# Kernel tuning notes

Hardware: AMD Instinct MI355X
Metric: run time of the kernel (lower is better)

Reference implementation:

```python
import jax, jax.numpy as jnp
import numpy as np

B, S, D, H = 16, 1024, 512, 8
DH = D // H
NEG = -2.0**32 + 1.0  # additive mask value used by the torch module

def leaky(x):
    return jnp.where(x >= 0, x, 0.2 * x)

def setup_inputs() -> dict:
    key = jax.random.key(0)
    ks = jax.random.split(key, 10)
    query = jax.random.normal(ks[0], (B, S, D), dtype=jnp.float32)
    key_t = jax.random.normal(ks[1], (B, S, D), dtype=jnp.float32)
    value = jax.random.normal(ks[2], (B, S, D), dtype=jnp.float32)
    q_mask = jax.random.randint(ks[3], (B, S), 0, 2).astype(jnp.float32)
    k_mask = jax.random.randint(ks[4], (B, S), 0, 2).astype(jnp.float32)
    # xavier-uniform-like linear weights [out, in], zero biases
    lim = float(np.sqrt(6.0 / (D + D)))
    WQ = jax.random.uniform(ks[5], (D, D), jnp.float32, -lim, lim)
    WK = jax.random.uniform(ks[6], (D, D), jnp.float32, -lim, lim)
    WV = jax.random.uniform(ks[7], (D, D), jnp.float32, -lim, lim)
    bQ = jnp.zeros((D,), jnp.float32)
    bK = jnp.zeros((D,), jnp.float32)
    bV = jnp.zeros((D,), jnp.float32)
    return {"query": query, "key": key_t, "value": value,
            "q_mask": q_mask, "k_mask": k_mask,
            "WQ": WQ, "bQ": bQ, "WK": WK, "bK": bK, "WV": WV, "bV": bV}

def reference(query, key, value, q_mask, k_mask, WQ, bQ, WK, bK, WV, bV):
    # projections + LeakyReLU(0.2)
    q = leaky(query @ WQ.T + bQ)   # [B,S,D]
    k = leaky(key   @ WK.T + bK)
    v = leaky(value @ WV.T + bV)
    # split heads: [B,S,D] -> [B,H,S,DH]
    q = q.reshape(B, S, H, DH).transpose(0, 2, 1, 3)
    k = k.reshape(B, S, H, DH).transpose(0, 2, 1, 3)
    v = v.reshape(B, S, H, DH).transpose(0, 2, 1, 3)
    # additive mask from outer product of masks (nonzero -> attend)
    pair = q_mask[:, :, None] * k_mask[:, None, :]          # [B,S,S]
    add_mask = jnp.where(pair != 0, 0.0, NEG)[:, None, :, :]  # [B,1,S,S]
    scores = jnp.einsum("bhqd,bhkd->bhqk", q, k)
    # NOTE: mask is added BEFORE scaling, matching torch.baddbmm then divide
    scores = (scores + add_mask) / jnp.sqrt(jnp.float32(DH))
    attn = jax.nn.softmax(scores, axis=-1)
    # post-softmax multiplicative query mask (dropout is identity in eval)
    attn = attn * q_mask[:, None, :, None]
    out = jnp.einsum("bhqk,bhkd->bhqd", attn, v)            # [B,H,S,DH]
    return out.transpose(0, 2, 1, 3).reshape(B, S, D)
```

## Files before the change

kernel.cpp:

```cpp
#include <hip/hip_runtime.h>
#include <hip/hip_bf16.h>


typedef __attribute__((ext_vector_type(4))) float  f32x4;
typedef __attribute__((ext_vector_type(8))) __bf16 bf16x8;
typedef __attribute__((ext_vector_type(4))) __bf16 bf16x4;
typedef __attribute__((ext_vector_type(4))) unsigned short u16x4;

#define DEVI static __device__ __forceinline__

DEVI unsigned short f2bf(float f) {
    unsigned u = __builtin_bit_cast(unsigned, f);
    unsigned r = u + 0x7fffu + ((u >> 16) & 1u);
    return (unsigned short)(r >> 16);
}

#define QSCALE 0.18033688011112042f

#define GLOAD16(g, l)                                                         \
    __builtin_amdgcn_global_load_lds(                                         \
        (const __attribute__((address_space(1))) void*)(g),                   \
        (__attribute__((address_space(3))) void*)(l), 16, 0, 0)

__global__ __launch_bounds__(256)
void prep_kernel(const float* __restrict__ qm, const float* __restrict__ km,
                 const float* __restrict__ WQ, const float* __restrict__ WK,
                 const float* __restrict__ WV,
                 int* __restrict__ nqv, int* __restrict__ nkv,
                 int* __restrict__ qidx, int* __restrict__ kidx,
                 int* __restrict__ zidx, unsigned short* __restrict__ Wb)
{
    if (blockIdx.x < 16) {
        if (threadIdx.x >= 128) return;
        const int b = blockIdx.x;
        const int w = threadIdx.x >> 6, l = threadIdx.x & 63;
        const float* msk = (w == 0 ? qm : km) + b * 1024;
        int* idx = (w == 0 ? qidx : kidx) + b * 1024;
        int cnt = 0;
        for (int i0 = 0; i0 < 1024; i0 += 64) {
            bool on = (msk[i0 + l] != 0.0f);
            unsigned long long bal = __ballot(on);
            int pre = cnt + (int)__popcll(bal & ((1ull << l) - 1ull));
            if (on) idx[pre] = i0 + l;
            else if (w == 0) zidx[b * 1024 + (i0 + l - pre)] = i0 + l;
            cnt += (int)__popcll(bal);
        }
        if (l == 0) *((w == 0 ? nqv : nkv) + b) = cnt;
        int pe = (cnt + 63) & ~63;
        for (int i = cnt + l; i < pe; i += 64) idx[i] = 0;
    } else {
        int i = (blockIdx.x - 16) * 256 + threadIdx.x;
        int m = i >> 16, j = i & 65535;
        const float* W = (m == 0) ? WQ : (m == 1) ? WK : WV;
        f32x4 v = *(const f32x4*)(W + (size_t)j * 4);
        u16x4 p = { f2bf(v[0]), f2bf(v[1]), f2bf(v[2]), f2bf(v[3]) };
        *(u16x4*)(Wb + (size_t)m * 262144 + (size_t)j * 4) = p;
    }
}

__global__ __launch_bounds__(256)
void proj_kernel(const float* __restrict__ Xq, const float* __restrict__ Xk,
                 const float* __restrict__ Xv, const unsigned short* __restrict__ Wb,
                 unsigned short* __restrict__ Qc, unsigned short* __restrict__ Kc,
                 unsigned short* __restrict__ VcT,
                 const int* __restrict__ nqv, const int* __restrict__ nkv,
                 const int* __restrict__ qidx, const int* __restrict__ kidx)
{
    __shared__ unsigned short lX[2][64 * 64];
    __shared__ unsigned short lW[2][128 * 64];

    const int z = blockIdx.y;
    const float* X = (z == 0) ? Xq : (z == 1) ? Xk : Xv;
    const unsigned short* Wz = Wb + (size_t)z * 262144;

    const int rb = blockIdx.x;
    const int xcd = rb & 7, inner = rb >> 3;
    const int b = ((inner & 1) << 3) | xcd;
    const int mt = (inner >> 1) & 15;
    const int nb = inner >> 5;
    const int n = (z == 0) ? nqv[b] : nkv[b];
    if (mt * 64 >= n) return;

    const int* ridx = ((z == 0) ? qidx : kidx) + b * 1024 + mt * 64;
    const float* Xb = X + (size_t)b * 1024 * 512;
    const int nbase = nb * 128;

    const int tid = threadIdx.x;
    const int w = tid >> 6, l = tid & 63, lg = l >> 4, cl = l & 15;
    const int wr = w >> 1, wc = w & 1;
    const int srow0 = tid >> 4, scol = tid & 15;
    const int wrow_in = l >> 3, wg0 = l & 7;

    f32x4 acc[2][4] = {};
    f32x4 xrA[4], xrB[4];

    int rg[4];
#pragma unroll
    for (int p = 0; p < 4; p++) {
        int rl = p * 16 + srow0;
        rg[p] = (mt * 64 + rl < n) ? ridx[rl] : 0;
    }

#define LOADX(dst, kb)                                                        \
    _Pragma("unroll")                                                         \
    for (int p = 0; p < 4; p++)                                               \
        dst[p] = *(const f32x4*)(Xb + (size_t)rg[p] * 512 + (kb) + scol * 4);
#define GLW(bn, kb)                                                           \
    _Pragma("unroll")                                                         \
    for (int it = 0; it < 4; it++) {                                          \
        int c = w * 4 + it;                                                   \
        int row = c * 8 + wrow_in;                                            \
        GLOAD16(Wz + (size_t)(nbase + row) * 512 + (kb) + (wg0 ^ (row & 7)) * 8, \
                (char*)lW[bn] + c * 1024);                                    \
    }
#define WRITEX(bn, src)                                                       \
    _Pragma("unroll")                                                         \
    for (int p = 0; p < 4; p++) {                                             \
        int row = p * 16 + srow0;                                             \
        bf16x4 px = { (__bf16)src[p][0], (__bf16)src[p][1],                   \
                      (__bf16)src[p][2], (__bf16)src[p][3] };                 \
        int off = (row * 128 + scol * 8) ^ ((row & 7) << 4);                  \
        *(bf16x4*)((char*)lX[bn] + off) = px;                                 \
    }
#define COMPUTE(bc)                                                           \
    _Pragma("unroll")                                                         \
    for (int ks = 0; ks < 2; ks++) {                                          \
        bf16x8 af[2], bfr[4];                                                 \
        _Pragma("unroll")                                                     \
        for (int mi = 0; mi < 2; mi++) {                                      \
            int row = wr * 32 + mi * 16 + cl;                                 \
            int off = (row * 128 + ks * 64 + lg * 16) ^ ((row & 7) << 4);     \
            af[mi] = *(const bf16x8*)((const char*)lX[bc] + off);             \
        }                                                                     \
        _Pragma("unroll")                                                     \
        for (int ni = 0; ni < 4; ni++) {                                      \
            int row = wc * 64 + ni * 16 + cl;                                 \
            int g = ks * 4 + lg;                                              \
            bfr[ni] = *(const bf16x8*)((const char*)lW[bc] + row * 128        \
                                       + ((g ^ (row & 7)) << 4));             \
        }                                                                     \
        _Pragma("unroll")                                                     \
        for (int mi = 0; mi < 2; mi++)                                        \
            _Pragma("unroll")                                                 \
            for (int ni = 0; ni < 4; ni++)                                    \
                acc[mi][ni] = __builtin_amdgcn_mfma_f32_16x16x32_bf16(        \
                    af[mi], bfr[ni], acc[mi][ni], 0, 0, 0);                   \
    }

    LOADX(xrA, 0);
    GLW(0, 0);
    WRITEX(0, xrA);
    __builtin_amdgcn_sched_barrier(0);
    LOADX(xrB, 64);
    asm volatile("s_waitcnt vmcnt(4) lgkmcnt(0)" ::: "memory");
    __builtin_amdgcn_s_barrier();

#pragma unroll
    for (int t = 0; t < 7; t++) {
        const int bc = t & 1, bn = bc ^ 1;
        GLW(bn, (t + 1) * 64);
        __builtin_amdgcn_sched_barrier(0);
        const int kx = ((t + 2 > 7) ? 7 : t + 2) * 64;
        if ((t & 1) == 0) { LOADX(xrA, kx); } else { LOADX(xrB, kx); }
        COMPUTE(bc);
        if ((t & 1) == 0) { WRITEX(bn, xrB); } else { WRITEX(bn, xrA); }
        asm volatile("s_waitcnt vmcnt(4) lgkmcnt(0)" ::: "memory");
        __builtin_amdgcn_s_barrier();
    }
    COMPUTE(1);

    if (z < 2) {
        unsigned short* O = (z == 0) ? Qc : Kc;
        const float qs = (z == 0) ? QSCALE : 1.0f;
#pragma unroll
        for (int mi = 0; mi < 2; mi++)
#pragma unroll
            for (int ni = 0; ni < 4; ni++) {
                int ocol = nbase + wc * 64 + ni * 16 + cl;
                int hh = ocol >> 6, dh = ocol & 63;
                unsigned short* Ob = O + (((size_t)b * 8 + hh) << 16) + dh;
                int j0 = mt * 64 + wr * 32 + mi * 16 + lg * 4;
#pragma unroll
                for (int r = 0; r < 4; r++) {
                    float v0 = acc[mi][ni][r];
                    v0 = fmaxf(v0, 0.2f * v0) * qs;
                    Ob[(size_t)(j0 + r) * 64] = f2bf(v0);
                }
            }
    } else {
#pragma unroll
        for (int mi = 0; mi < 2; mi++)
#pragma unroll
            for (int ni = 0; ni < 4; ni++) {
                int ocol = nbase + wc * 64 + ni * 16 + cl;
                int hh = ocol >> 6, dh = ocol & 63;
                unsigned short* Ob = VcT + (((size_t)b * 8 + hh) * 64 + dh) * 1024;
                int j0 = mt * 64 + wr * 32 + mi * 16 + lg * 4;
                u16x4 pk;
#pragma unroll
                for (int r = 0; r < 4; r++) {
                    float v0 = acc[mi][ni][r];
                    v0 = fmaxf(v0, 0.2f * v0);
                    pk[r] = f2bf(v0);
                }
                *(u16x4*)(Ob + j0) = pk;
            }
    }
#undef LOADX
#undef GLW
#undef WRITEX
#undef COMPUTE
}

__global__ __launch_bounds__(128)
void attn_kernel(const unsigned short* __restrict__ Qc, const unsigned short* __restrict__ Kc,
                 const unsigned short* __restrict__ VcT, const int* __restrict__ nqv,
                 const int* __restrict__ nkv, const int* __restrict__ qidx,
                 const int* __restrict__ zidx, float* __restrict__ out)
{
    __shared__ unsigned short lK[2][4096];
    __shared__ unsigned short lV[2][4096];
    __shared__ char Pl[2][4096];

    const int tid = threadIdx.x;
    const int f0 = blockIdx.x;

    if (f0 >= 2048) {
        const int idx = f0 - 2048;
        const int zb = idx >> 6, chunk = idx & 63;
        const int nz = 1024 - nqv[zb];
        const int r = chunk * 16 + (tid >> 3);
        if (r < nz) {
            const int zr = zidx[zb * 1024 + r];
            float* o = out + ((size_t)zb * 1024 + zr) * 512 + (tid & 7) * 64;
            f32x4 zv = {};
#pragma unroll
            for (int i = 0; i < 16; i++) *(f32x4*)(o + i * 4) = zv;
        }
        return;
    }

    const int w = tid >> 6, l = tid & 63, lg = l >> 4, cl = l & 15;
    const int xcd = f0 & 7, inner = f0 >> 3;
    const int qb = inner >> 4;
    const int bh = xcd * 16 + (inner & 15);
    const int b = bh >> 3, h = bh & 7;
    const int nq = nqv[b], nk = nkv[b];
    if (qb * 64 >= nq) return;
    const int q0 = qb * 64 + w * 32;
    const unsigned short* Qb = Qc + ((size_t)bh << 16);
    const unsigned short* Kb = Kc + ((size_t)bh << 16);
    const unsigned short* Vb = VcT + ((size_t)bh << 16);

    bf16x8 qa[2][2];
#pragma unroll
    for (int u = 0; u < 2; u++) {
        int qr = q0 + u * 16 + cl; if (qr > nq - 1) qr = nq - 1;
        qa[u][0] = *(const bf16x8*)(Qb + (size_t)qr * 64 + lg * 8);
        qa[u][1] = *(const bf16x8*)(Qb + (size_t)qr * 64 + 32 + lg * 8);
    }
    const bf16x8 ones = { (__bf16)1.0f, (__bf16)1.0f, (__bf16)1.0f, (__bf16)1.0f,
                          (__bf16)1.0f, (__bf16)1.0f, (__bf16)1.0f, (__bf16)1.0f };

    f32x4 acc[4][2] = {};
    f32x4 accS[2] = {};
    const int ntile = (nk + 63) >> 6;
    const int wboff = ((lg >> 1) << 8) | (cl << 4) | ((lg & 1) << 3);
    const int srow8 = l >> 3;
    const int sgx = ((l & 7) ^ srow8) * 8;

#define STAGEKV(bn, kt_) { const int k0s = (kt_) << 6;                        \
    _Pragma("unroll")                                                         \
    for (int it = 0; it < 4; it++) {                                          \
        int c = w * 4 + it;                                                   \
        int row = c * 8 + srow8;                                              \
        GLOAD16(Kb + (size_t)(k0s + row) * 64 + sgx, (char*)lK[bn] + c * 1024); \
        GLOAD16(Vb + (size_t)row * 1024 + k0s + sgx, (char*)lV[bn] + c * 1024); \
    } }

    STAGEKV(0, 0);
    __syncthreads();

    for (int kt = 0; kt < ntile; kt++) {
        const int bc = kt & 1;
        if (kt + 1 < ntile) STAGEKV(bc ^ 1, kt + 1);
        const int k0 = kt << 6;
        const char* Kl = (const char*)lK[bc];
        const char* Vl = (const char*)lV[bc];
        char* Pb = &Pl[w][0];
        f32x4 sc[4][2];
        __builtin_amdgcn_s_setprio(1);
#pragma unroll
        for (int t = 0; t < 4; t++) {
            int kr = t * 16 + cl;
            int sw = (kr & 7) << 4;
            bf16x8 kb0 = *(const bf16x8*)(Kl + ((kr * 128 + lg * 16) ^ sw));
            bf16x8 kb1 = *(const bf16x8*)(Kl + ((kr * 128 + (lg + 4) * 16) ^ sw));
#pragma unroll
            for (int u = 0; u < 2; u++) {
                f32x4 zz = {};
                zz = __builtin_amdgcn_mfma_f32_16x16x32_bf16(kb0, qa[u][0], zz, 0, 0, 0);
                sc[t][u] = __builtin_amdgcn_mfma_f32_16x16x32_bf16(kb1, qa[u][1], zz, 0, 0, 0);
            }
        }
        __builtin_amdgcn_s_setprio(0);
        const bool tail = (k0 + 64 > nk);
#pragma unroll
        for (int u = 0; u < 2; u++)
#pragma unroll
            for (int t = 0; t < 4; t++) {
                float lt0 = sc[t][u][0], lt1 = sc[t][u][1];
                float lt2 = sc[t][u][2], lt3 = sc[t][u][3];
                if (tail) {
                    int kbase = k0 + t * 16 + lg * 4;
                    if (kbase + 0 >= nk) lt0 = -3e38f;
                    if (kbase + 1 >= nk) lt1 = -3e38f;
                    if (kbase + 2 >= nk) lt2 = -3e38f;
                    if (kbase + 3 >= nk) lt3 = -3e38f;
                }
                float p0 = __builtin_amdgcn_exp2f(lt0);
                float p1 = __builtin_amdgcn_exp2f(lt1);
                float p2 = __builtin_amdgcn_exp2f(lt2);
                float p3 = __builtin_amdgcn_exp2f(lt3);
                bf16x4 pk = { (__bf16)p0, (__bf16)p1, (__bf16)p2, (__bf16)p3 };
                *(bf16x4*)(Pb + u * 2048 + t * 512 + wboff) = pk;
            }
        bf16x8 pa[2][2];
#pragma unroll
        for (int u = 0; u < 2; u++) {
            pa[u][0] = *(const bf16x8*)(Pb + u * 2048 + l * 16);
            pa[u][1] = *(const bf16x8*)(Pb + u * 2048 + 1024 + l * 16);
        }
        __builtin_amdgcn_s_setprio(1);
#pragma unroll
        for (int f = 0; f < 4; f++) {
            int vr = f * 16 + cl;
            int sw = (vr & 7) << 4;
            bf16x8 vb0 = *(const bf16x8*)(Vl + ((vr * 128 + lg * 16) ^ sw));
            bf16x8 vb1 = *(const bf16x8*)(Vl + ((vr * 128 + (lg + 4) * 16) ^ sw));
#pragma unroll
            for (int u = 0; u < 2; u++) {
                acc[f][u] = __builtin_amdgcn_mfma_f32_16x16x32_bf16(vb0, pa[u][0], acc[f][u], 0, 0, 0);
                acc[f][u] = __builtin_amdgcn_mfma_f32_16x16x32_bf16(vb1, pa[u][1], acc[f][u], 0, 0, 0);
            }
        }
#pragma unroll
        for (int u = 0; u < 2; u++) {
            accS[u] = __builtin_amdgcn_mfma_f32_16x16x32_bf16(ones, pa[u][0], accS[u], 0, 0, 0);
            accS[u] = __builtin_amdgcn_mfma_f32_16x16x32_bf16(ones, pa[u][1], accS[u], 0, 0, 0);
        }
        __builtin_amdgcn_s_setprio(0);
        __syncthreads();
    }

#pragma unroll
    for (int u = 0; u < 2; u++) {
        if (q0 + u * 16 + cl < nq) {
            const float inv = 1.0f / accS[u][0];
            const int qq = qidx[b * 1024 + q0 + u * 16 + cl];
            float* orow = out + ((size_t)b * 1024 + qq) * 512 + h * 64 + lg * 4;
#pragma unroll
            for (int f = 0; f < 4; f++) {
                f32x4 o = { acc[f][u][0] * inv, acc[f][u][1] * inv,
                            acc[f][u][2] * inv, acc[f][u][3] * inv };
                *(f32x4*)(orow + f * 16) = o;
            }
        }
    }
}

extern "C" void kernel_launch(void* const* d_in, const int* in_sizes, int n_in,
                              void* d_out, int out_size, void* d_ws, size_t ws_size,
                              hipStream_t stream)
{
    const float* q   = (const float*)d_in[0];
    const float* k   = (const float*)d_in[1];
    const float* v   = (const float*)d_in[2];
    const float* qm  = (const float*)d_in[3];
    const float* kmk = (const float*)d_in[4];
    const float* WQ  = (const float*)d_in[5];
    const float* WK  = (const float*)d_in[7];
    const float* WV  = (const float*)d_in[9];

    const size_t perT = (size_t)16 * 8 * 1024 * 64;
    unsigned short* Qc  = (unsigned short*)d_ws;
    unsigned short* Kc  = Qc + perT;
    unsigned short* VcT = Kc + perT;
    int* nqv  = (int*)(VcT + perT);
    int* nkv  = nqv + 16;
    int* qidx = nkv + 16;
    int* kidx = qidx + 16384;
    int* zidx = kidx + 16384;
    unsigned short* Wb = (unsigned short*)(zidx + 16384);
    float* out = (float*)d_out;

    prep_kernel<<<784, 256, 0, stream>>>(qm, kmk, WQ, WK, WV,
                                         nqv, nkv, qidx, kidx, zidx, Wb);
    proj_kernel<<<dim3(1024, 3), 256, 0, stream>>>(q, k, v, Wb, Qc, Kc, VcT,
                                                   nqv, nkv, qidx, kidx);
    attn_kernel<<<3072, 128, 0, stream>>>(Qc, Kc, VcT, nqv, nkv, qidx, zidx, out);
}
```

Before: 82.85 us.

## Split attention block into four waves of 16 query rows each

```diff
diff --git a/kernel.cpp b/kernel.cpp
--- a/kernel.cpp
+++ b/kernel.cpp
@@ -212,7 +212,7 @@
 #undef COMPUTE
 }
 
-__global__ __launch_bounds__(128)
+__global__ __launch_bounds__(256)
 void attn_kernel(const unsigned short* __restrict__ Qc, const unsigned short* __restrict__ Kc,
                  const unsigned short* __restrict__ VcT, const int* __restrict__ nqv,
                  const int* __restrict__ nkv, const int* __restrict__ qidx,
@@ -220,16 +220,16 @@
 {
     __shared__ unsigned short lK[2][4096];
     __shared__ unsigned short lV[2][4096];
-    __shared__ char Pl[2][4096];
+    __shared__ char Pl[4][2048];
 
     const int tid = threadIdx.x;
     const int f0 = blockIdx.x;
 
     if (f0 >= 2048) {
         const int idx = f0 - 2048;
-        const int zb = idx >> 6, chunk = idx & 63;
+        const int zb = idx >> 5, chunk = idx & 31;
         const int nz = 1024 - nqv[zb];
-        const int r = chunk * 16 + (tid >> 3);
+        const int r = chunk * 32 + (tid >> 3);
         if (r < nz) {
             const int zr = zidx[zb * 1024 + r];
             float* o = out + ((size_t)zb * 1024 + zr) * 512 + (tid & 7) * 64;
@@ -247,23 +247,22 @@
     const int b = bh >> 3, h = bh & 7;
     const int nq = nqv[b], nk = nkv[b];
     if (qb * 64 >= nq) return;
-    const int q0 = qb * 64 + w * 32;
+    const int q0 = qb * 64 + w * 16;
     const unsigned short* Qb = Qc + ((size_t)bh << 16);
     const unsigned short* Kb = Kc + ((size_t)bh << 16);
     const unsigned short* Vb = VcT + ((size_t)bh << 16);
 
-    bf16x8 qa[2][2];
-#pragma unroll
-    for (int u = 0; u < 2; u++) {
-        int qr = q0 + u * 16 + cl; if (qr > nq - 1) qr = nq - 1;
-        qa[u][0] = *(const bf16x8*)(Qb + (size_t)qr * 64 + lg * 8);
-        qa[u][1] = *(const bf16x8*)(Qb + (size_t)qr * 64 + 32 + lg * 8);
+    bf16x8 qa0, qa1;
+    {
+        int qr = q0 + cl; if (qr > nq - 1) qr = nq - 1;
+        qa0 = *(const bf16x8*)(Qb + (size_t)qr * 64 + lg * 8);
+        qa1 = *(const bf16x8*)(Qb + (size_t)qr * 64 + 32 + lg * 8);
     }
     const bf16x8 ones = { (__bf16)1.0f, (__bf16)1.0f, (__bf16)1.0f, (__bf16)1.0f,
                           (__bf16)1.0f, (__bf16)1.0f, (__bf16)1.0f, (__bf16)1.0f };
 
-    f32x4 acc[4][2] = {};
-    f32x4 accS[2] = {};
+    f32x4 acc[4] = {};
+    f32x4 accS = {};
     const int ntile = (nk + 63) >> 6;
     const int wboff = ((lg >> 1) << 8) | (cl << 4) | ((lg & 1) << 3);
     const int srow8 = l >> 3;
@@ -271,8 +270,8 @@
 
 #define STAGEKV(bn, kt_) { const int k0s = (kt_) << 6;                        \
     _Pragma("unroll")                                                         \
-    for (int it = 0; it < 4; it++) {                                          \
-        int c = w * 4 + it;                                                   \
+    for (int it = 0; it < 2; it++) {                                          \
+        int c = w * 2 + it;                                                   \
         int row = c * 8 + srow8;                                              \
         GLOAD16(Kb + (size_t)(k0s + row) * 64 + sgx, (char*)lK[bn] + c * 1024); \
         GLOAD16(Vb + (size_t)row * 1024 + k0s + sgx, (char*)lV[bn] + c * 1024); \
@@ -288,7 +287,7 @@
         const char* Kl = (const char*)lK[bc];
         const char* Vl = (const char*)lV[bc];
         char* Pb = &Pl[w][0];
-        f32x4 sc[4][2];
+        f32x4 sc[4];
         __builtin_amdgcn_s_setprio(1);
 #pragma unroll
         for (int t = 0; t < 4; t++) {
@@ -296,41 +295,32 @@
             int sw = (kr & 7) << 4;
             bf16x8 kb0 = *(const bf16x8*)(Kl + ((kr * 128 + lg * 16) ^ sw));
             bf16x8 kb1 = *(const bf16x8*)(Kl + ((kr * 128 + (lg + 4) * 16) ^ sw));
-#pragma unroll
-            for (int u = 0; u < 2; u++) {
-                f32x4 zz = {};
-                zz = __builtin_amdgcn_mfma_f32_16x16x32_bf16(kb0, qa[u][0], zz, 0, 0, 0);
-                sc[t][u] = __builtin_amdgcn_mfma_f32_16x16x32_bf16(kb1, qa[u][1], zz, 0, 0, 0);
-            }
+            f32x4 zz = {};
+            zz    = __builtin_amdgcn_mfma_f32_16x16x32_bf16(kb0, qa0, zz, 0, 0, 0);
+            sc[t] = __builtin_amdgcn_mfma_f32_16x16x32_bf16(kb1, qa1, zz, 0, 0, 0);
         }
         __builtin_amdgcn_s_setprio(0);
         const bool tail = (k0 + 64 > nk);
 #pragma unroll
-        for (int u = 0; u < 2; u++)
-#pragma unroll
-            for (int t = 0; t < 4; t++) {
-                float lt0 = sc[t][u][0], lt1 = sc[t][u][1];
-                float lt2 = sc[t][u][2], lt3 = sc[t][u][3];
-                if (tail) {
-                    int kbase = k0 + t * 16 + lg * 4;
-                    if (kbase + 0 >= nk) lt0 = -3e38f;
-                    if (kbase + 1 >= nk) lt1 = -3e38f;
-                    if (kbase + 2 >= nk) lt2 = -3e38f;
-                    if (kbase + 3 >= nk) lt3 = -3e38f;
-                }
-                float p0 = __builtin_amdgcn_exp2f(lt0);
-                float p1 = __builtin_amdgcn_exp2f(lt1);
-                float p2 = __builtin_amdgcn_exp2f(lt2);
-                float p3 = __builtin_amdgcn_exp2f(lt3);
-                bf16x4 pk = { (__bf16)p0, (__bf16)p1, (__bf16)p2, (__bf16)p3 };
-                *(bf16x4*)(Pb + u * 2048 + t * 512 + wboff) = pk;
+        for (int t = 0; t < 4; t++) {
+            float lt0 = sc[t][0], lt1 = sc[t][1];
+            float lt2 = sc[t][2], lt3 = sc[t][3];
+            if (tail) {
+                int kbase = k0 + t * 16 + lg * 4;
+                if (kbase + 0 >= nk) lt0 = -3e38f;
+                if (kbase + 1 >= nk) lt1 = -3e38f;
+                if (kbase + 2 >= nk) lt2 = -3e38f;
+                if (kbase + 3 >= nk) lt3 = -3e38f;
             }
-        bf16x8 pa[2][2];
-#pragma unroll
-        for (int u = 0; u < 2; u++) {
-            pa[u][0] = *(const bf16x8*)(Pb + u * 2048 + l * 16);
-            pa[u][1] = *(const bf16x8*)(Pb + u * 2048 + 1024 + l * 16);
-        }
+            float p0 = __builtin_amdgcn_exp2f(lt0);
+            float p1 = __builtin_amdgcn_exp2f(lt1);
+            float p2 = __builtin_amdgcn_exp2f(lt2);
+            float p3 = __builtin_amdgcn_exp2f(lt3);
+            bf16x4 pk = { (__bf16)p0, (__bf16)p1, (__bf16)p2, (__bf16)p3 };
+            *(bf16x4*)(Pb + t * 512 + wboff) = pk;
+        }
+        bf16x8 pa0 = *(const bf16x8*)(Pb + l * 16);
+        bf16x8 pa1 = *(const bf16x8*)(Pb + 1024 + l * 16);
         __builtin_amdgcn_s_setprio(1);
 #pragma unroll
         for (int f = 0; f < 4; f++) {
@@ -338,33 +328,24 @@
             int sw = (vr & 7) << 4;
             bf16x8 vb0 = *(const bf16x8*)(Vl + ((vr * 128 + lg * 16) ^ sw));
             bf16x8 vb1 = *(const bf16x8*)(Vl + ((vr * 128 + (lg + 4) * 16) ^ sw));
-#pragma unroll
-            for (int u = 0; u < 2; u++) {
-                acc[f][u] = __builtin_amdgcn_mfma_f32_16x16x32_bf16(vb0, pa[u][0], acc[f][u], 0, 0, 0);
-                acc[f][u] = __builtin_amdgcn_mfma_f32_16x16x32_bf16(vb1, pa[u][1], acc[f][u], 0, 0, 0);
-            }
-        }
-#pragma unroll
-        for (int u = 0; u < 2; u++) {
-            accS[u] = __builtin_amdgcn_mfma_f32_16x16x32_bf16(ones, pa[u][0], accS[u], 0, 0, 0);
-            accS[u] = __builtin_amdgcn_mfma_f32_16x16x32_bf16(ones, pa[u][1], accS[u], 0, 0, 0);
-        }
+            acc[f] = __builtin_amdgcn_mfma_f32_16x16x32_bf16(vb0, pa0, acc[f], 0, 0, 0);
+            acc[f] = __builtin_amdgcn_mfma_f32_16x16x32_bf16(vb1, pa1, acc[f], 0, 0, 0);
+        }
+        accS = __builtin_amdgcn_mfma_f32_16x16x32_bf16(ones, pa0, accS, 0, 0, 0);
+        accS = __builtin_amdgcn_mfma_f32_16x16x32_bf16(ones, pa1, accS, 0, 0, 0);
         __builtin_amdgcn_s_setprio(0);
         __syncthreads();
     }
 
-#pragma unroll
-    for (int u = 0; u < 2; u++) {
-        if (q0 + u * 16 + cl < nq) {
-            const float inv = 1.0f / accS[u][0];
-            const int qq = qidx[b * 1024 + q0 + u * 16 + cl];
-            float* orow = out + ((size_t)b * 1024 + qq) * 512 + h * 64 + lg * 4;
-#pragma unroll
-            for (int f = 0; f < 4; f++) {
-                f32x4 o = { acc[f][u][0] * inv, acc[f][u][1] * inv,
-                            acc[f][u][2] * inv, acc[f][u][3] * inv };
-                *(f32x4*)(orow + f * 16) = o;
-            }
+    if (q0 + cl < nq) {
+        const float inv = 1.0f / accS[0];
+        const int qq = qidx[b * 1024 + q0 + cl];
+        float* orow = out + ((size_t)b * 1024 + qq) * 512 + h * 64 + lg * 4;
+#pragma unroll
+        for (int f = 0; f < 4; f++) {
+            f32x4 o = { acc[f][0] * inv, acc[f][1] * inv,
+                        acc[f][2] * inv, acc[f][3] * inv };
+            *(f32x4*)(orow + f * 16) = o;
         }
     }
 }
@@ -398,5 +379,5 @@
                                          nqv, nkv, qidx, kidx, zidx, Wb);
     proj_kernel<<<dim3(1024, 3), 256, 0, stream>>>(q, k, v, Wb, Qc, Kc, VcT,
                                                    nqv, nkv, qidx, kidx);
-    attn_kernel<<<3072, 128, 0, stream>>>(Qc, Kc, VcT, nqv, nkv, qidx, zidx, out);
-}
+    attn_kernel<<<2560, 256, 0, stream>>>(Qc, Kc, VcT, nqv, nkv, qidx, zidx, out);
+}
```

New measurement: 78.19 us (median of 3 runs). 1.06x faster.
